# Kernel optimization log

Hardware: AMD Instinct MI355X
Metric: run time of the kernel (lower is better)

The kernel has to match this reference:

```python
import jax, jax.numpy as jnp
import numpy as np

PPU = 64          # points_per_unit
MARGIN = 0.1
INIT_LENGTHSCALE = 0.1


def setup_inputs() -> dict:
    key = jax.random.key(0)
    k1, k2, k3 = jax.random.split(key, 3)
    m, nc, nt, dim, dy = 8, 1024, 512, 2, 2
    xc = jax.random.uniform(k1, (m, nc, dim), jnp.float32)
    yc = jax.random.normal(k2, (m, nc, dy), jnp.float32)
    xt = jax.random.uniform(k3, (m, nt, dim), jnp.float32)
    # lengthscale_param = log(exp(init_ls) - 1) so softplus(param) == init_ls
    lengthscale_param = jnp.log(jnp.expm1(jnp.full((dim,), INIT_LENGTHSCALE, jnp.float32)))
    return {"xc": xc, "yc": yc, "xt": xt, "lengthscale_param": lengthscale_param}


def reference(xc, yc, xt, lengthscale_param):
    m, _, dim = xc.shape
    lengthscale = 1e-5 + jax.nn.softplus(lengthscale_param)  # (dim,)

    # append density channel of ones
    yc1 = jnp.concatenate([yc, jnp.ones(yc.shape[:-1] + (1,), yc.dtype)], axis=-1)

    # adaptive grid over concat(xc, xt)
    x_all = jnp.concatenate([xc, xt], axis=-2)
    xmin = x_all.min(axis=-2)  # (m, dim)
    xmax = x_all.max(axis=-2)  # (m, dim)
    Nf = jnp.ceil((0.5 * (xmax - xmin) + MARGIN) * PPU).max(axis=0)
    Nf = 2.0 ** jnp.ceil(jnp.log2(Nf))
    N = np.asarray(Nf).astype(np.int64)  # concrete per-dim half-widths (grid size)

    axes = [jnp.arange(-int(n), int(n) + 1, dtype=xc.dtype) for n in N]  # inclusive, like torch.range
    base = jnp.stack(jnp.meshgrid(*axes, indexing='ij'), axis=-1)  # (n1,...,ndim, dim)
    x_mid = 0.5 * (xmin + xmax)  # (m, dim)
    x_grid = x_mid.reshape((m,) + (1,) * dim + (dim,)) + base[None] / PPU  # (m, n1,...,ndim, dim)
    x_grid_flat = x_grid.reshape(m, -1, dim)  # (m, ng, dim)

    # RBF weights: exp(-0.5 * ||(g - c)/ls||^2) via expanded quadratic form
    a = x_grid_flat / lengthscale  # (m, ng, dim)
    b = xc / lengthscale           # (m, nc, dim)
    dist2 = ((a * a).sum(-1)[:, :, None]
             + (b * b).sum(-1)[:, None, :]
             - 2.0 * jnp.einsum('bgd,bcd->bgc', a, b))
    weights = jnp.exp(-0.5 * jnp.maximum(dist2, 0.0))  # (m, ng, nc)

    z_flat = weights @ yc1  # (m, ng, dy+1)
    z_grid = z_flat.reshape(x_grid.shape[:-1] + (yc1.shape[-1],))
    return (x_grid, z_grid)
```

## Files before the change

### kernel.cpp

```cpp
#include <hip/hip_runtime.h>
#include <math.h>

#define M_BATCH 8
#define NC 1024
#define NTGT 512
#define G_DIM 129
#define NG (G_DIM * G_DIM)
#define N_OUT (G_DIM * 3)
#define TM 32
#define TIY 32
#define KCH 128
#define NKCH (NC / KCH)
#define LDA 136
#define ABYTES (TM * LDA * 2)
#define BUFBYTES (2 * ABYTES + 512)
#define GT 5

typedef __attribute__((ext_vector_type(8))) _Float16 half8;
typedef __attribute__((ext_vector_type(2))) _Float16 half2v;
typedef __attribute__((ext_vector_type(4))) float floatx4;

#if defined(__has_builtin)
#if __has_builtin(__builtin_amdgcn_exp2f)
#define FAST_EXP2(x) __builtin_amdgcn_exp2f(x)
#endif
#endif
#ifndef FAST_EXP2
#define FAST_EXP2(x) exp2f(x)
#endif

__global__ __launch_bounds__(512) void fused_kernel(
        const float* __restrict__ xc, const float* __restrict__ yc,
        const float* __restrict__ xt, const float* __restrict__ lsp,
        float* __restrict__ out_grid, float* __restrict__ out_z) {
    const int tid = threadIdx.x;
    const int iyt = blockIdx.x;
    const int mt = blockIdx.y;
    const int m  = blockIdx.z;

    __shared__ __align__(16) char lds_raw[2 * BUFBYTES];

    {
        float mn0 = 1e30f, mx0 = -1e30f, mn1 = 1e30f, mx1 = -1e30f;
        const float2* pc = (const float2*)(xc + m * NC * 2);
        for (int i = tid; i < NC; i += 512) {
            float2 p = pc[i];
            mn0 = fminf(mn0, p.x); mx0 = fmaxf(mx0, p.x);
            mn1 = fminf(mn1, p.y); mx1 = fmaxf(mx1, p.y);
        }
        const float2* pt = (const float2*)(xt + m * NTGT * 2);
        {
            float2 p = pt[tid];
            mn0 = fminf(mn0, p.x); mx0 = fmaxf(mx0, p.x);
            mn1 = fminf(mn1, p.y); mx1 = fmaxf(mx1, p.y);
        }
        ((float4*)lds_raw)[tid] = make_float4(mn0, mx0, mn1, mx1);
    }
    __syncthreads();
    {
        float4* sm = (float4*)lds_raw;
        for (int s = 256; s > 0; s >>= 1) {
            if (tid < s) {
                float4 a = sm[tid], b = sm[tid + s];
                sm[tid] = make_float4(fminf(a.x, b.x), fmaxf(a.y, b.y),
                                      fminf(a.z, b.z), fmaxf(a.w, b.w));
            }
            __syncthreads();
        }
    }
    const float mid0 = 0.5f * (((float4*)lds_raw)[0].x + ((float4*)lds_raw)[0].y);
    const float mid1 = 0.5f * (((float4*)lds_raw)[0].z + ((float4*)lds_raw)[0].w);
    __syncthreads();

    const float Kc = 0.84932180028801904272f;
    const float ls0 = 1e-5f + log1pf(expf(lsp[0]));
    const float ls1 = 1e-5f + log1pf(expf(lsp[1]));
    const float s0 = Kc / ls0, s1 = Kc / ls1;
    const float inv_ppu = 1.0f / 64.0f;

    if (iyt == 0) {
        const int r0 = mt * TM;
        const int nrows = min(TM, G_DIM - r0);
        float2* og = (float2*)out_grid + (size_t)m * NG;
        for (int g = tid; g < nrows * G_DIM; g += 512) {
            const int r = g / G_DIM;
            const int iyy = g - r * G_DIM;
            const int ixg = r0 + r;
            og[(size_t)ixg * G_DIM + iyy] =
                make_float2(mid0 + (float)(ixg - 64) * inv_ppu,
                            mid1 + (float)(iyy - 64) * inv_ppu);
        }
    }

    const int c2 = (tid & 63) * 2;
    const int r0s = tid >> 6;
    const float4* xc4 = (const float4*)(xc + m * NC * 2);
    const float4* yc4 = (const float4*)(yc + m * NC * 2);
    const float gxs_base = (mid0 + (float)(mt * TM - 64) * inv_ppu) * s0;
    const float gys_base = (mid1 + (float)(iyt * TIY - 64) * inv_ppu) * s1;
    const float gstep_x = inv_ppu * s0;
    const float gstep_y = inv_ppu * s1;

    const int w = tid >> 6;
    const int g = w >> 2;
    const int wm = (w >> 1) & 1;
    const int wn = w & 1;
    const int lane = tid & 63;
    const int ln = lane & 15;
    const int q = lane >> 4;

    floatx4 acc0 = {0.f, 0.f, 0.f, 0.f};
    floatx4 acc1 = {0.f, 0.f, 0.f, 0.f};
    floatx4 acc2 = {0.f, 0.f, 0.f, 0.f};

    auto stage = [&](int kc, int buf) {
        const int cp = kc * 64 + (tid & 63);
        const float4 xq = xc4[cp];
        const float4 yq = yc4[cp];
        const float cx0 = xq.x * s0, cx1 = xq.z * s0;
        const float cy0 = xq.y * s1, cy1 = xq.w * s1;
        _Float16* Ab  = (_Float16*)(lds_raw + buf * BUFBYTES);
        _Float16* Wyb = (_Float16*)(lds_raw + buf * BUFBYTES + ABYTES);
        _Float16* yeb = (_Float16*)(lds_raw + buf * BUFBYTES + 2 * ABYTES);
        _Float16* yob = yeb + 128;
#pragma unroll
        for (int i = 0; i < 4; ++i) {
            const int r = r0s + 8 * i;
            const float gxs = gxs_base + (float)r * gstep_x;
            const float dx0 = gxs - cx0;
            const float dx1 = gxs - cx1;
            *(half2v*)&Ab[r * LDA + c2] =
                (half2v){(_Float16)FAST_EXP2(-(dx0 * dx0)),
                         (_Float16)FAST_EXP2(-(dx1 * dx1))};
            const float gys = gys_base + (float)r * gstep_y;
            const float dy0 = gys - cy0;
            const float dy1 = gys - cy1;
            *(half2v*)&Wyb[r * LDA + c2] =
                (half2v){(_Float16)FAST_EXP2(-(dy0 * dy0)),
                         (_Float16)FAST_EXP2(-(dy1 * dy1))};
        }
        if (tid < 64) {
            *(half2v*)&yeb[c2] = (half2v){(_Float16)yq.x, (_Float16)yq.z};
            *(half2v*)&yob[c2] = (half2v){(_Float16)yq.y, (_Float16)yq.w};
        }
    };

    stage(0, 0);
    __syncthreads();

    for (int kc = 0; kc < NKCH; ++kc) {
        const int buf = kc & 1;
        const _Float16* Ab  = (const _Float16*)(lds_raw + buf * BUFBYTES);
        const _Float16* Wyb = (const _Float16*)(lds_raw + buf * BUFBYTES + ABYTES);
        const _Float16* yeb = (const _Float16*)(lds_raw + buf * BUFBYTES + 2 * ABYTES);
#pragma unroll
        for (int kk = 0; kk < 2; ++kk) {
            const int off = g * 64 + kk * 32 + q * 8;
            half8 a  = *(const half8*)&Ab[(wm * 16 + ln) * LDA + off];
            half8 wy = *(const half8*)&Wyb[(wn * 16 + ln) * LDA + off];
            half8 ye = *(const half8*)&yeb[off];
            half8 yo = *(const half8*)&yeb[128 + off];
            acc2 = __builtin_amdgcn_mfma_f32_16x16x32_f16(a, wy, acc2, 0, 0, 0);
            acc0 = __builtin_amdgcn_mfma_f32_16x16x32_f16(a, wy * ye, acc0, 0, 0, 0);
            acc1 = __builtin_amdgcn_mfma_f32_16x16x32_f16(a, wy * yo, acc1, 0, 0, 0);
        }
        if (kc + 1 < NKCH) stage(kc + 1, buf ^ 1);
        __syncthreads();
    }

    floatx4* cs = (floatx4*)lds_raw;
    const int ws = wm * 2 + wn;
    if (g == 1) {
        cs[(ws * 3 + 0) * 64 + lane] = acc0;
        cs[(ws * 3 + 1) * 64 + lane] = acc1;
        cs[(ws * 3 + 2) * 64 + lane] = acc2;
    }
    __syncthreads();
    if (g == 0) {
        const floatx4 o0 = cs[(ws * 3 + 0) * 64 + lane];
        const floatx4 o1 = cs[(ws * 3 + 1) * 64 + lane];
        const floatx4 o2 = cs[(ws * 3 + 2) * 64 + lane];
        const int iyg = iyt * TIY + wn * 16 + ln;
        if (iyg < G_DIM) {
            float* oz = out_z + (size_t)m * NG * 3 + (size_t)iyg * 3;
            const int ixb = mt * TM + wm * 16 + q * 4;
#pragma unroll
            for (int rr = 0; rr < 4; ++rr) {
                const int ixg = ixb + rr;
                if (ixg < G_DIM) {
                    float* p = oz + (size_t)ixg * N_OUT;
                    p[0] = acc0[rr] + o0[rr];
                    p[1] = acc1[rr] + o1[rr];
                    p[2] = acc2[rr] + o2[rr];
                }
            }
        }
    }
}

extern "C" void kernel_launch(void* const* d_in, const int* in_sizes, int n_in,
                              void* d_out, int out_size, void* d_ws, size_t ws_size,
                              hipStream_t stream) {
    const float* xc  = (const float*)d_in[0];
    const float* yc  = (const float*)d_in[1];
    const float* xt  = (const float*)d_in[2];
    const float* lsp = (const float*)d_in[3];

    float* out_grid = (float*)d_out;
    float* out_z = out_grid + (size_t)M_BATCH * NG * 2;

    dim3 grid(GT, GT, M_BATCH);
    fused_kernel<<<grid, 512, 0, stream>>>(xc, yc, xt, lsp, out_grid, out_z);
}
```

Before: 67.86 us.

## Split min/max into a separate kernel and retile grid to 16x16 blocks

The per-batch min/max reduction moves out of the fused kernel into a small pre-kernel that writes grid midpoints to workspace, so each tile block no longer repeats the reduction. The fused kernel changes to 16x16 output tiles with 256 threads and 256-wide K chunks, raising block count from 200 to 648. Each of the four waves takes a K slice and the partial accumulators are combined in LDS. The smaller tiles recompute the separable exp weights with less sharing per block, and the extra launch adds some overhead.

New measurement: 71.00 us. +4.6%, slower.

```diff
diff --git a/kernel.cpp b/kernel.cpp
--- a/kernel.cpp
+++ b/kernel.cpp
@@ -7,14 +7,14 @@
 #define G_DIM 129
 #define NG (G_DIM * G_DIM)
 #define N_OUT (G_DIM * 3)
-#define TM 32
-#define TIY 32
-#define KCH 128
+#define TM 16
+#define TIY 16
+#define KCH 256
 #define NKCH (NC / KCH)
-#define LDA 136
+#define LDA 264
 #define ABYTES (TM * LDA * 2)
-#define BUFBYTES (2 * ABYTES + 512)
-#define GT 5
+#define BUFBYTES (2 * ABYTES + 1024)
+#define GT 9
 
 typedef __attribute__((ext_vector_type(8))) _Float16 half8;
 typedef __attribute__((ext_vector_type(2))) _Float16 half2v;
@@ -29,9 +29,50 @@
 #define FAST_EXP2(x) exp2f(x)
 #endif
 
-__global__ __launch_bounds__(512) void fused_kernel(
+__global__ __launch_bounds__(256) void minmax_kernel(
+        const float* __restrict__ xc, const float* __restrict__ xt,
+        float* __restrict__ ws) {
+    const int m = blockIdx.x;
+    const int tid = threadIdx.x;
+    float mn0 = 1e30f, mx0 = -1e30f, mn1 = 1e30f, mx1 = -1e30f;
+    const float2* pc = (const float2*)(xc + m * NC * 2);
+    for (int i = tid; i < NC; i += 256) {
+        float2 p = pc[i];
+        mn0 = fminf(mn0, p.x); mx0 = fmaxf(mx0, p.x);
+        mn1 = fminf(mn1, p.y); mx1 = fmaxf(mx1, p.y);
+    }
+    const float2* pt = (const float2*)(xt + m * NTGT * 2);
+    for (int i = tid; i < NTGT; i += 256) {
+        float2 p = pt[i];
+        mn0 = fminf(mn0, p.x); mx0 = fmaxf(mx0, p.x);
+        mn1 = fminf(mn1, p.y); mx1 = fmaxf(mx1, p.y);
+    }
+#pragma unroll
+    for (int s = 1; s < 64; s <<= 1) {
+        mn0 = fminf(mn0, __shfl_xor(mn0, s));
+        mx0 = fmaxf(mx0, __shfl_xor(mx0, s));
+        mn1 = fminf(mn1, __shfl_xor(mn1, s));
+        mx1 = fmaxf(mx1, __shfl_xor(mx1, s));
+    }
+    __shared__ float4 red[4];
+    if ((tid & 63) == 0) red[tid >> 6] = make_float4(mn0, mx0, mn1, mx1);
+    __syncthreads();
+    if (tid == 0) {
+        float4 a = red[0];
+#pragma unroll
+        for (int w2 = 1; w2 < 4; ++w2) {
+            float4 b = red[w2];
+            a.x = fminf(a.x, b.x); a.y = fmaxf(a.y, b.y);
+            a.z = fminf(a.z, b.z); a.w = fmaxf(a.w, b.w);
+        }
+        ws[2 * m]     = 0.5f * (a.x + a.y);
+        ws[2 * m + 1] = 0.5f * (a.z + a.w);
+    }
+}
+
+__global__ __launch_bounds__(256) void fused_kernel(
         const float* __restrict__ xc, const float* __restrict__ yc,
-        const float* __restrict__ xt, const float* __restrict__ lsp,
+        const float* __restrict__ lsp, const float* __restrict__ ws,
         float* __restrict__ out_grid, float* __restrict__ out_z) {
     const int tid = threadIdx.x;
     const int iyt = blockIdx.x;
@@ -40,37 +81,8 @@
 
     __shared__ __align__(16) char lds_raw[2 * BUFBYTES];
 
-    {
-        float mn0 = 1e30f, mx0 = -1e30f, mn1 = 1e30f, mx1 = -1e30f;
-        const float2* pc = (const float2*)(xc + m * NC * 2);
-        for (int i = tid; i < NC; i += 512) {
-            float2 p = pc[i];
-            mn0 = fminf(mn0, p.x); mx0 = fmaxf(mx0, p.x);
-            mn1 = fminf(mn1, p.y); mx1 = fmaxf(mx1, p.y);
-        }
-        const float2* pt = (const float2*)(xt + m * NTGT * 2);
-        {
-            float2 p = pt[tid];
-            mn0 = fminf(mn0, p.x); mx0 = fmaxf(mx0, p.x);
-            mn1 = fminf(mn1, p.y); mx1 = fmaxf(mx1, p.y);
-        }
-        ((float4*)lds_raw)[tid] = make_float4(mn0, mx0, mn1, mx1);
-    }
-    __syncthreads();
-    {
-        float4* sm = (float4*)lds_raw;
-        for (int s = 256; s > 0; s >>= 1) {
-            if (tid < s) {
-                float4 a = sm[tid], b = sm[tid + s];
-                sm[tid] = make_float4(fminf(a.x, b.x), fmaxf(a.y, b.y),
-                                      fminf(a.z, b.z), fmaxf(a.w, b.w));
-            }
-            __syncthreads();
-        }
-    }
-    const float mid0 = 0.5f * (((float4*)lds_raw)[0].x + ((float4*)lds_raw)[0].y);
-    const float mid1 = 0.5f * (((float4*)lds_raw)[0].z + ((float4*)lds_raw)[0].w);
-    __syncthreads();
+    const float mid0 = ws[2 * m];
+    const float mid1 = ws[2 * m + 1];
 
     const float Kc = 0.84932180028801904272f;
     const float ls0 = 1e-5f + log1pf(expf(lsp[0]));
@@ -82,7 +94,7 @@
         const int r0 = mt * TM;
         const int nrows = min(TM, G_DIM - r0);
         float2* og = (float2*)out_grid + (size_t)m * NG;
-        for (int g = tid; g < nrows * G_DIM; g += 512) {
+        for (int g = tid; g < nrows * G_DIM; g += 256) {
             const int r = g / G_DIM;
             const int iyy = g - r * G_DIM;
             const int ixg = r0 + r;
@@ -92,8 +104,9 @@
         }
     }
 
-    const int c2 = (tid & 63) * 2;
-    const int r0s = tid >> 6;
+    const int cpair = tid & 127;
+    const int rbase = tid >> 7;
+    const int c2 = cpair * 2;
     const float4* xc4 = (const float4*)(xc + m * NC * 2);
     const float4* yc4 = (const float4*)(yc + m * NC * 2);
     const float gxs_base = (mid0 + (float)(mt * TM - 64) * inv_ppu) * s0;
@@ -102,9 +115,6 @@
     const float gstep_y = inv_ppu * s1;
 
     const int w = tid >> 6;
-    const int g = w >> 2;
-    const int wm = (w >> 1) & 1;
-    const int wn = w & 1;
     const int lane = tid & 63;
     const int ln = lane & 15;
     const int q = lane >> 4;
@@ -114,7 +124,7 @@
     floatx4 acc2 = {0.f, 0.f, 0.f, 0.f};
 
     auto stage = [&](int kc, int buf) {
-        const int cp = kc * 64 + (tid & 63);
+        const int cp = kc * 128 + cpair;
         const float4 xq = xc4[cp];
         const float4 yq = yc4[cp];
         const float cx0 = xq.x * s0, cx1 = xq.z * s0;
@@ -122,10 +132,10 @@
         _Float16* Ab  = (_Float16*)(lds_raw + buf * BUFBYTES);
         _Float16* Wyb = (_Float16*)(lds_raw + buf * BUFBYTES + ABYTES);
         _Float16* yeb = (_Float16*)(lds_raw + buf * BUFBYTES + 2 * ABYTES);
-        _Float16* yob = yeb + 128;
-#pragma unroll
-        for (int i = 0; i < 4; ++i) {
-            const int r = r0s + 8 * i;
+        _Float16* yob = yeb + KCH;
+#pragma unroll
+        for (int i = 0; i < 8; ++i) {
+            const int r = rbase + 2 * i;
             const float gxs = gxs_base + (float)r * gstep_x;
             const float dx0 = gxs - cx0;
             const float dx1 = gxs - cx1;
@@ -139,7 +149,7 @@
                 (half2v){(_Float16)FAST_EXP2(-(dy0 * dy0)),
                          (_Float16)FAST_EXP2(-(dy1 * dy1))};
         }
-        if (tid < 64) {
+        if (tid < 128) {
             *(half2v*)&yeb[c2] = (half2v){(_Float16)yq.x, (_Float16)yq.z};
             *(half2v*)&yob[c2] = (half2v){(_Float16)yq.y, (_Float16)yq.w};
         }
@@ -155,11 +165,11 @@
         const _Float16* yeb = (const _Float16*)(lds_raw + buf * BUFBYTES + 2 * ABYTES);
 #pragma unroll
         for (int kk = 0; kk < 2; ++kk) {
-            const int off = g * 64 + kk * 32 + q * 8;
-            half8 a  = *(const half8*)&Ab[(wm * 16 + ln) * LDA + off];
-            half8 wy = *(const half8*)&Wyb[(wn * 16 + ln) * LDA + off];
+            const int off = (w * 2 + kk) * 32 + q * 8;
+            half8 a  = *(const half8*)&Ab[ln * LDA + off];
+            half8 wy = *(const half8*)&Wyb[ln * LDA + off];
             half8 ye = *(const half8*)&yeb[off];
-            half8 yo = *(const half8*)&yeb[128 + off];
+            half8 yo = *(const half8*)&yeb[KCH + off];
             acc2 = __builtin_amdgcn_mfma_f32_16x16x32_f16(a, wy, acc2, 0, 0, 0);
             acc0 = __builtin_amdgcn_mfma_f32_16x16x32_f16(a, wy * ye, acc0, 0, 0, 0);
             acc1 = __builtin_amdgcn_mfma_f32_16x16x32_f16(a, wy * yo, acc1, 0, 0, 0);
@@ -169,29 +179,31 @@
     }
 
     floatx4* cs = (floatx4*)lds_raw;
-    const int ws = wm * 2 + wn;
-    if (g == 1) {
-        cs[(ws * 3 + 0) * 64 + lane] = acc0;
-        cs[(ws * 3 + 1) * 64 + lane] = acc1;
-        cs[(ws * 3 + 2) * 64 + lane] = acc2;
+    if (w > 0) {
+        cs[((w - 1) * 3 + 0) * 64 + lane] = acc0;
+        cs[((w - 1) * 3 + 1) * 64 + lane] = acc1;
+        cs[((w - 1) * 3 + 2) * 64 + lane] = acc2;
     }
     __syncthreads();
-    if (g == 0) {
-        const floatx4 o0 = cs[(ws * 3 + 0) * 64 + lane];
-        const floatx4 o1 = cs[(ws * 3 + 1) * 64 + lane];
-        const floatx4 o2 = cs[(ws * 3 + 2) * 64 + lane];
-        const int iyg = iyt * TIY + wn * 16 + ln;
+    if (w == 0) {
+#pragma unroll
+        for (int ww = 0; ww < 3; ++ww) {
+            acc0 += cs[(ww * 3 + 0) * 64 + lane];
+            acc1 += cs[(ww * 3 + 1) * 64 + lane];
+            acc2 += cs[(ww * 3 + 2) * 64 + lane];
+        }
+        const int iyg = iyt * TIY + ln;
         if (iyg < G_DIM) {
             float* oz = out_z + (size_t)m * NG * 3 + (size_t)iyg * 3;
-            const int ixb = mt * TM + wm * 16 + q * 4;
+            const int ixb = mt * TM + q * 4;
 #pragma unroll
             for (int rr = 0; rr < 4; ++rr) {
                 const int ixg = ixb + rr;
                 if (ixg < G_DIM) {
                     float* p = oz + (size_t)ixg * N_OUT;
-                    p[0] = acc0[rr] + o0[rr];
-                    p[1] = acc1[rr] + o1[rr];
-                    p[2] = acc2[rr] + o2[rr];
+                    p[0] = acc0[rr];
+                    p[1] = acc1[rr];
+                    p[2] = acc2[rr];
                 }
             }
         }
@@ -208,7 +220,10 @@
 
     float* out_grid = (float*)d_out;
     float* out_z = out_grid + (size_t)M_BATCH * NG * 2;
+    float* ws = (float*)d_ws;
+
+    minmax_kernel<<<dim3(M_BATCH), 256, 0, stream>>>(xc, xt, ws);
 
     dim3 grid(GT, GT, M_BATCH);
-    fused_kernel<<<grid, 512, 0, stream>>>(xc, yc, xt, lsp, out_grid, out_z);
+    fused_kernel<<<grid, 256, 0, stream>>>(xc, yc, lsp, ws, out_grid, out_z);
 }
```
